# Optimization experiments

Hardware: AMD Instinct MI355X
Metric: run time of the kernel (lower is better)

The kernel has to match this reference:

```python
import jax, jax.numpy as jnp
import numpy as np

NUM_NODES = 20000
NUM_EDGES = 1_000_000
NUM_REL = 12        # internal num_relation (init arg 24 // 2)
NUM_STEP = 6
HID = 128
B_SET = 64          # number of unique (h, r) queries
BS, NEG = 64, 32    # scoring batch
EPS = 1e-10


def setup_inputs() -> dict:
    key = jax.random.key(0)
    ks = jax.random.split(key, 16)
    s = 0.1
    inp = {
        "query_emb": jax.random.normal(ks[0], (2 * NUM_REL + 1, HID), jnp.float32) * s,
        "w_ih": jax.random.normal(ks[1], (4 * HID, HID), jnp.float32) * s,
        "w_hh": jax.random.normal(ks[2], (4 * HID, HID), jnp.float32) * s,
        "b_ih": jax.random.normal(ks[3], (4 * HID,), jnp.float32) * s,
        "b_hh": jax.random.normal(ks[4], (4 * HID,), jnp.float32) * s,
        "wl_w": jax.random.normal(ks[5], (2 * NUM_REL, HID), jnp.float32) * s,
        "wl_b": jax.random.normal(ks[6], (2 * NUM_REL,), jnp.float32) * s,
        "lin_w": jax.random.normal(ks[7], (1, 1), jnp.float32),
        "lin_b": jax.random.normal(ks[8], (1,), jnp.float32),
        "edge_index": jax.random.randint(ks[9], (2, NUM_EDGES), 0, NUM_NODES, jnp.int64),
        "edge_type": jax.random.randint(ks[10], (NUM_EDGES,), 0, 2 * NUM_REL, jnp.int64),
        "h_set": jax.random.randint(ks[11], (B_SET,), 0, NUM_NODES, jnp.int64),
        "r_set": jax.random.randint(ks[12], (B_SET,), 0, NUM_REL, jnp.int64),
        "t_index": jax.random.randint(ks[13], (BS, NEG), 0, NUM_NODES, jnp.int64),
        "hr_inverse": jax.random.randint(ks[14], (BS, NEG), 0, B_SET, jnp.int64),
    }
    return inp


def _lstm(query, w_ih, w_hh, b_ih, b_hh):
    # query: [T, B, D]; single-layer PyTorch LSTM (gate order i, f, g, o)
    B, D = query.shape[1], w_hh.shape[1]
    h0 = jnp.zeros((B, D), query.dtype)

    def step(carry, x):
        h, c = carry
        gates = x @ w_ih.T + b_ih + h @ w_hh.T + b_hh
        i, f, g, o = jnp.split(gates, 4, axis=-1)
        c = jax.nn.sigmoid(f) * c + jax.nn.sigmoid(i) * jnp.tanh(g)
        h = jax.nn.sigmoid(o) * jnp.tanh(c)
        return (h, c), h

    _, hidden = jax.lax.scan(step, (h0, h0), query)
    return hidden  # [T, B, D]


def reference(query_emb, w_ih, w_hh, b_ih, b_hh, wl_w, wl_b, lin_w, lin_b,
              edge_index, edge_type, h_set, r_set, t_index, hr_inverse):
    N1 = NUM_NODES + 1
    B = h_set.shape[0]
    # query sequence: relation repeated (T-1) times, then END token (= NUM_REL)
    q_index = jnp.concatenate(
        [jnp.tile(r_set[None, :], (NUM_STEP - 1, 1)),
         jnp.full((1, B), NUM_REL, dtype=r_set.dtype)], axis=0)  # [T, B]
    query = query_emb[q_index]                                   # [T, B, D]
    hidden = _lstm(query, w_ih, w_hh, b_ih, b_hh)                # [T, B, D]

    memory = jax.nn.one_hot(h_set, N1, dtype=query_emb.dtype)[None]  # [1, B, N1]
    node_in, node_out = edge_index[0], edge_index[1]

    output = None
    for i in range(NUM_STEP):
        k = hidden[i]                 # [B, D]
        v = hidden[: i + 1]           # [i+1, B, D]
        attn = jax.nn.softmax(jnp.einsum('bd,tbd->bt', k, v), axis=-1)
        inp = jnp.einsum('bt,tbn->nb', attn, memory)             # [N1, B]
        weight = jax.nn.softmax(k @ wl_w.T + wl_b, axis=-1).T    # [2R, B]
        # gather -> weight -> scatter_add over edges (edge_weight == 1)
        message = inp[node_in] * weight[edge_type]               # [E, B]
        output = jax.ops.segment_sum(message, node_out, num_segments=N1)
        output = output / jnp.maximum(output.sum(0, keepdims=True), EPS)
        memory = jnp.concatenate([memory, output.T[None]], axis=0)

    score = output[t_index, hr_inverse]           # [BS, NEG]
    return score * lin_w[0, 0] + lin_b[0]
```

## Files before the change

### kernel.cpp

```cpp
#include <hip/hip_runtime.h>
#include <hip/hip_fp16.h>
#include <math.h>

namespace {

constexpr int kN1 = 20001;
constexpr int kNE = 1000000;
constexpr int kNStep = 6;
constexpr int kHid = 128;
constexpr int kB = 64;
constexpr int kNRel2 = 24;
constexpr float kEps = 1e-10f;
constexpr unsigned kSent = (unsigned)kN1;
constexpr int kPMax = kNE + 8 * kN1;
constexpr int kGatherBlocks = 2048;
constexpr int kNWaves = kGatherBlocks * 4;

__device__ __forceinline__ float sig(float x) { return 1.0f / (1.0f + expf(-x)); }

__device__ __forceinline__ float2 cvt2(unsigned u) {
  __half2 h = *reinterpret_cast<__half2*>(&u);
  return __half22float2(h);
}


__global__ __launch_bounds__(256) void transpose_w_kernel(
    const float* __restrict__ w_ih, const float* __restrict__ w_hh,
    float* __restrict__ wt) {
  const int idx = blockIdx.x * 256 + threadIdx.x;
  if (idx < 256 * 512) {
    const int k = idx >> 9;
    const int j = idx & 511;
    wt[idx] = (k < 128) ? w_ih[j * kHid + k] : w_hh[j * kHid + (k - 128)];
  }
}

__global__ __launch_bounds__(512) void lstm_fast_kernel(
    const float* __restrict__ query_emb, const float* __restrict__ wt,
    const float* __restrict__ b_ih, const float* __restrict__ b_hh,
    const int* __restrict__ r_set, float* __restrict__ hidden ) {
  const int b = blockIdx.x;
  const int tid = threadIdx.x;
  __shared__ float xh[256];
  __shared__ float cst[kHid];
  __shared__ float gsm[512];
  const float bias = b_ih[tid] + b_hh[tid];
  const int q = r_set[b];
  if (tid < kHid) { cst[tid] = 0.f; xh[kHid + tid] = 0.f; }
  for (int s = 0; s < kNStep; ++s) {
    if (tid < kHid) xh[tid] = query_emb[((s < kNStep - 1) ? q : 12) * kHid + tid];
    __syncthreads();
    float acc = bias;
#pragma unroll 8
    for (int k = 0; k < 256; ++k) acc += xh[k] * wt[k * 512 + tid];
    gsm[tid] = acc;
    __syncthreads();
    if (tid < kHid) {
      const float ig = sig(gsm[tid]);
      const float fg = sig(gsm[kHid + tid]);
      const float gg = tanhf(gsm[2 * kHid + tid]);
      const float og = sig(gsm[3 * kHid + tid]);
      const float cn = fg * cst[tid] + ig * gg;
      cst[tid] = cn;
      const float hn = og * tanhf(cn);
      xh[kHid + tid] = hn;
      hidden[(s * kB + b) * kHid + tid] = hn;
    }
    __syncthreads();
  }
}

__global__ __launch_bounds__(256) void lstm_kernel(
    const float* __restrict__ query_emb, const float* __restrict__ w_ih,
    const float* __restrict__ w_hh, const float* __restrict__ b_ih,
    const float* __restrict__ b_hh, const int* __restrict__ r_set,
    float* __restrict__ hidden) {
  const int b = blockIdx.x;
  const int tid = threadIdx.x;
  __shared__ float xs[kHid], hs[kHid], cs[kHid], gates[4 * kHid];
  if (tid < kHid) { hs[tid] = 0.f; cs[tid] = 0.f; }
  __syncthreads();
  for (int s = 0; s < kNStep; ++s) {
    const int q = (s < kNStep - 1) ? r_set[b] : 12;
    if (tid < kHid) xs[tid] = query_emb[q * kHid + tid];
    __syncthreads();
    for (int j = tid; j < 4 * kHid; j += blockDim.x) {
      const float* wi = &w_ih[j * kHid];
      const float* wh = &w_hh[j * kHid];
      float a = b_ih[j] + b_hh[j];
#pragma unroll 4
      for (int k = 0; k < kHid; ++k) a += xs[k] * wi[k] + hs[k] * wh[k];
      gates[j] = a;
    }
    __syncthreads();
    if (tid < kHid) {
      const float ig = sig(gates[tid]);
      const float fg = sig(gates[kHid + tid]);
      const float gg = tanhf(gates[2 * kHid + tid]);
      const float og = sig(gates[3 * kHid + tid]);
      const float cn = fg * cs[tid] + ig * gg;
      const float hn = og * tanhf(cn);
      cs[tid] = cn;
      hs[tid] = hn;
      hidden[(s * kB + b) * kHid + tid] = hn;
    }
    __syncthreads();
  }
}

__global__ __launch_bounds__(128) void attn_weight_kernel(
    const float* __restrict__ hidden, const float* __restrict__ wl_w,
    const float* __restrict__ wl_b, float* __restrict__ attnAll ,
    float* __restrict__ weightAll ) {
  const int b = blockIdx.x;
  const int tid = threadIdx.x;
  __shared__ float hsm[kNStep][kHid];
  __shared__ float G[kNStep][kNStep];
  __shared__ float logits[kNStep][kNRel2];
  for (int s = 0; s < kNStep; ++s) hsm[s][tid] = hidden[(s * kB + b) * kHid + tid];
  __syncthreads();
  if (tid < 36) {
    const int i = tid / 6, t = tid % 6;
    if (t <= i) {
      float acc = 0.f;
      for (int k = 0; k < kHid; ++k) acc += hsm[i][k] * hsm[t][k];
      G[i][t] = acc;
    }
  }
  for (int p = tid; p < kNStep * kNRel2; p += 128) {
    const int i = p / kNRel2, r = p % kNRel2;
    float acc = wl_b[r];
    for (int k = 0; k < kHid; ++k) acc += hsm[i][k] * wl_w[r * kHid + k];
    logits[i][r] = acc;
  }
  __syncthreads();
  if (tid < kNStep) {
    const int i = tid;
    float m = G[i][0];
    for (int t = 1; t <= i; ++t) m = fmaxf(m, G[i][t]);
    float ssum = 0.f;
    float ev[kNStep];
    for (int t = 0; t <= i; ++t) { ev[t] = expf(G[i][t] - m); ssum += ev[t]; }
    for (int t = 0; t <= i; ++t) attnAll[(i * kNStep + t) * kB + b] = ev[t] / ssum;
    float mw = logits[i][0];
    for (int r = 1; r < kNRel2; ++r) mw = fmaxf(mw, logits[i][r]);
    float sw = 0.f;
    float ew[kNRel2];
    for (int r = 0; r < kNRel2; ++r) { ew[r] = expf(logits[i][r] - mw); sw += ew[r]; }
    for (int r = 0; r < kNRel2; ++r) weightAll[(i * kNRel2 + r) * kB + b] = ew[r] / sw;
  }
}


__global__ __launch_bounds__(256) void zero_kernel(int* __restrict__ counts,
                                                   float* __restrict__ colsumAll) {
  const int i = blockIdx.x * blockDim.x + threadIdx.x;
  if (i < kN1) counts[i] = 0;
  if (i < kNStep * kB) colsumAll[i] = 0.f;
}

__global__ __launch_bounds__(256) void hist_kernel(const int* __restrict__ nout,
                                                   int* __restrict__ counts) {
  for (int e = blockIdx.x * blockDim.x + threadIdx.x; e < kNE;
       e += gridDim.x * blockDim.x)
    atomicAdd(&counts[nout[e]], 1);
}

__global__ __launch_bounds__(1024) void scan_kernel(const int* __restrict__ counts,
                                                    int* __restrict__ poffsets,
                                                    int* __restrict__ cursor) {
  __shared__ int part[1024];
  const int tid = threadIdx.x;
  const int chunk = (kN1 + 1023) / 1024;
  const int beg = tid * chunk;
  const int end = min(beg + chunk, kN1);
  int s = 0;
  for (int i = beg; i < end; ++i) s += (counts[i] + 7) & ~7;
  part[tid] = s;
  __syncthreads();
  for (int off = 1; off < 1024; off <<= 1) {
    const int v = (tid >= off) ? part[tid - off] : 0;
    __syncthreads();
    part[tid] += v;
    __syncthreads();
  }
  int run = part[tid] - s;
  for (int i = beg; i < end; ++i) {
    poffsets[i] = run;
    cursor[i] = run;
    run += (counts[i] + 7) & ~7;
  }
  if (tid == 1023) poffsets[kN1] = part[1023];
}

__global__ __launch_bounds__(256) void fill_kernel(unsigned* __restrict__ packed) {
  for (int i = blockIdx.x * blockDim.x + threadIdx.x; i < kPMax;
       i += gridDim.x * blockDim.x)
    packed[i] = kSent;
}

__global__ __launch_bounds__(256) void permute_kernel(
    const int* __restrict__ nin, const int* __restrict__ nout,
    const int* __restrict__ etype, int* __restrict__ cursor,
    unsigned* __restrict__ packed) {
  for (int e = blockIdx.x * blockDim.x + threadIdx.x; e < kNE;
       e += gridDim.x * blockDim.x) {
    const int d = nout[e];
    const int pos = atomicAdd(&cursor[d], 1);
    packed[pos] = (unsigned)nin[e] | ((unsigned)etype[e] << 15);
  }
}


__global__ __launch_bounds__(256) void inp_kernel(
    const float* __restrict__ attnAll, const float* __restrict__ colsumAll,
    const int* __restrict__ h_set, const float* __restrict__ outs,
    __half* __restrict__ inp, int step) {
  __shared__ float coef[kNStep][kB];
  __shared__ int hsm[kB];
  const int tid = threadIdx.x;
  for (int j = tid; j < kNStep * kB; j += 256) {
    const int t = j >> 6, b = j & 63;
    float c = 0.f;
    if (t == 0)
      c = attnAll[(step * kNStep) * kB + b];
    else if (t <= step)
      c = attnAll[(step * kNStep + t) * kB + b] /
          fmaxf(colsumAll[(t - 1) * kB + b], kEps);
    coef[t][b] = c;
  }
  if (tid < kB) hsm[tid] = h_set[tid];
  __syncthreads();
  const int total = (kN1 + 1) * 16;
  for (int idx = blockIdx.x * blockDim.x + tid; idx < total;
       idx += gridDim.x * blockDim.x) {
    const int n = idx >> 4;
    const int cg = idx & 15;
    float ax = 0.f, ay = 0.f, az = 0.f, aw = 0.f;
    if (n < kN1) {
      for (int t = 1; t <= step; ++t) {
        const float4 ct = *reinterpret_cast<const float4*>(&coef[t][cg * 4]);
        const float4 o = *reinterpret_cast<const float4*>(
            &outs[((long long)(t - 1) * kN1 + n) * kB + cg * 4]);
        ax += ct.x * o.x; ay += ct.y * o.y; az += ct.z * o.z; aw += ct.w * o.w;
      }
      const int c0 = cg * 4;
      if (hsm[c0 + 0] == n) ax += coef[0][c0 + 0];
      if (hsm[c0 + 1] == n) ay += coef[0][c0 + 1];
      if (hsm[c0 + 2] == n) az += coef[0][c0 + 2];
      if (hsm[c0 + 3] == n) aw += coef[0][c0 + 3];
    }
    __half2 h0 = __floats2half2_rn(ax, ay);
    __half2 h1 = __floats2half2_rn(az, aw);
    uint2 u;
    u.x = *reinterpret_cast<unsigned*>(&h0);
    u.y = *reinterpret_cast<unsigned*>(&h1);
    *reinterpret_cast<uint2*>(inp + (long long)idx * 4) = u;
  }
}

__global__ __launch_bounds__(256) void gather_seg_kernel(
    const __half* __restrict__ inp ,
    const float* __restrict__ weight ,
    const unsigned* __restrict__ packed, const int* __restrict__ poffsets,
    float* __restrict__ out, float* __restrict__ colsum) {
  __shared__ __align__(16) __half wsm[kNRel2 * kB];
  __shared__ float red[4][kB];
  const int tid = threadIdx.x;
  const int lane = tid & 63;
  const int wid = tid >> 6;
  const int g = lane >> 3;
  const int cb = lane & 7;
  for (int j = tid; j < kNRel2 * kB; j += 256) wsm[j] = __float2half(weight[j]);
  __syncthreads();

  float csum[8] = {0.f, 0.f, 0.f, 0.f, 0.f, 0.f, 0.f, 0.f};
  float acc[8] = {0.f, 0.f, 0.f, 0.f, 0.f, 0.f, 0.f, 0.f};

  auto flushNode = [&](int node) {
#pragma unroll
    for (int j = 0; j < 8; ++j) {
      acc[j] += __shfl_xor(acc[j], 8);
      acc[j] += __shfl_xor(acc[j], 16);
      acc[j] += __shfl_xor(acc[j], 32);
    }
    if (g == 0) {
      *reinterpret_cast<float4*>(out + (long long)node * kB + cb * 8) =
          make_float4(acc[0], acc[1], acc[2], acc[3]);
      *reinterpret_cast<float4*>(out + (long long)node * kB + cb * 8 + 4) =
          make_float4(acc[4], acc[5], acc[6], acc[7]);
#pragma unroll
      for (int j = 0; j < 8; ++j) csum[j] += acc[j];
    }
#pragma unroll
    for (int j = 0; j < 8; ++j) acc[j] = 0.f;
  };

  const int wave = blockIdx.x * 4 + wid;
  const int P = poffsets[kN1];
  const int nG = P >> 3;
  const int chunkG = (nG + kNWaves - 1) / kNWaves;
  const int gbeg = wave * chunkG;
  if (gbeg < nG) {
    const int gend = min(gbeg + chunkG, nG);
    auto lb = [&](int x) {
      int lo = 0, hi = kN1;
      while (lo < hi) {
        const int mid = (lo + hi) >> 1;
        if (poffsets[mid] < x) lo = mid + 1; else hi = mid;
      }
      return lo;
    };
    const int nbeg = lb(gbeg * 8);
    const int nend = (gend >= nG) ? kN1 : lb(gend * 8);
    if (nbeg < nend) {
      int n = nbeg;
      int nextB = poffsets[n + 1];
      const int ebeg = poffsets[nbeg];
      const int eend = poffsets[nend];
      unsigned pA = (ebeg < eend) ? packed[ebeg + g] : kSent;
      unsigned pB = (ebeg + 8 < eend) ? packed[ebeg + 8 + g] : kSent;
      uint4 vA = *reinterpret_cast<const uint4*>(
          inp + (long long)(pA & 0x7fffu) * kB + cb * 8);
      uint4 vB = *reinterpret_cast<const uint4*>(
          inp + (long long)(pB & 0x7fffu) * kB + cb * 8);
      for (int ebase = ebeg; ebase < eend; ebase += 16) {
        const bool hasB = (ebase + 8) < eend;
        const int e2 = ebase + 16, e3 = ebase + 24;
        const unsigned pC = (e2 < eend) ? packed[e2 + g] : kSent;
        const unsigned pD = (e3 < eend) ? packed[e3 + g] : kSent;
        while (ebase >= nextB) { flushNode(n); ++n; nextB = poffsets[n + 1]; }
        {
          const uint4 w4 =
              *reinterpret_cast<const uint4*>(wsm + (pA >> 15) * kB + cb * 8);
          const float2 v0 = cvt2(vA.x), v1 = cvt2(vA.y), v2 = cvt2(vA.z), v3 = cvt2(vA.w);
          const float2 w0 = cvt2(w4.x), w1 = cvt2(w4.y), w2 = cvt2(w4.z), w3 = cvt2(w4.w);
          acc[0] += v0.x * w0.x; acc[1] += v0.y * w0.y;
          acc[2] += v1.x * w1.x; acc[3] += v1.y * w1.y;
          acc[4] += v2.x * w2.x; acc[5] += v2.y * w2.y;
          acc[6] += v3.x * w3.x; acc[7] += v3.y * w3.y;
        }
        if (hasB) {
          while (ebase + 8 >= nextB) { flushNode(n); ++n; nextB = poffsets[n + 1]; }
          const uint4 w4 =
              *reinterpret_cast<const uint4*>(wsm + (pB >> 15) * kB + cb * 8);
          const float2 v0 = cvt2(vB.x), v1 = cvt2(vB.y), v2 = cvt2(vB.z), v3 = cvt2(vB.w);
          const float2 w0 = cvt2(w4.x), w1 = cvt2(w4.y), w2 = cvt2(w4.z), w3 = cvt2(w4.w);
          acc[0] += v0.x * w0.x; acc[1] += v0.y * w0.y;
          acc[2] += v1.x * w1.x; acc[3] += v1.y * w1.y;
          acc[4] += v2.x * w2.x; acc[5] += v2.y * w2.y;
          acc[6] += v3.x * w3.x; acc[7] += v3.y * w3.y;
        }
        pA = pC; pB = pD;
        vA = *reinterpret_cast<const uint4*>(
            inp + (long long)(pC & 0x7fffu) * kB + cb * 8);
        vB = *reinterpret_cast<const uint4*>(
            inp + (long long)(pD & 0x7fffu) * kB + cb * 8);
      }
      while (n < nend) { flushNode(n); ++n; }
    }
  }
  if (g == 0) {
#pragma unroll
    for (int j = 0; j < 8; ++j) red[wid][cb * 8 + j] = csum[j];
  }
  __syncthreads();
  if (wid == 0) {
    const float r = red[0][lane] + red[1][lane] + red[2][lane] + red[3][lane];
    unsafeAtomicAdd(&colsum[lane], r);
  }
}

__global__ __launch_bounds__(256) void score_kernel(
    const float* __restrict__ outLast, const float* __restrict__ colsumLast,
    const int* __restrict__ t_index, const int* __restrict__ hr_inverse,
    const float* __restrict__ lin_w, const float* __restrict__ lin_b,
    float* __restrict__ out, int n) {
  const int i = blockIdx.x * blockDim.x + threadIdx.x;
  if (i < n) {
    const int node = t_index[i];
    const int b = hr_inverse[i];
    const float v = outLast[(long long)node * kB + b] / fmaxf(colsumLast[b], kEps);
    out[i] = v * lin_w[0] + lin_b[0];
  }
}


__global__ __launch_bounds__(256) void inp_zero_kernel(
    const float* __restrict__ attnAll, const int* __restrict__ h_set,
    const float* __restrict__ outs, float* __restrict__ inp,
    float* __restrict__ out_next, float* __restrict__ colsum, int step) {
  const long long total = (long long)kN1 * kB;
  for (long long idx = (long long)blockIdx.x * blockDim.x + threadIdx.x; idx < total;
       idx += (long long)gridDim.x * blockDim.x) {
    const int b = (int)(idx & 63);
    const int n = (int)(idx >> 6);
    float acc = (h_set[b] == n) ? attnAll[(step * kNStep) * kB + b] : 0.f;
    for (int t = 1; t <= step; ++t)
      acc += attnAll[(step * kNStep + t) * kB + b] *
             outs[(long long)(t - 1) * kN1 * kB + idx];
    inp[idx] = acc;
    out_next[idx] = 0.f;
  }
  if (blockIdx.x == 0 && threadIdx.x < kB) colsum[threadIdx.x] = 0.f;
}

__global__ __launch_bounds__(256) void scatter_kernel(
    const float* __restrict__ inp, const float* __restrict__ weight,
    const int* __restrict__ nin, const int* __restrict__ nout,
    const int* __restrict__ etype, float* __restrict__ out,
    float* __restrict__ colsum) {
  const int lane = threadIdx.x & 63;
  const int wave = blockIdx.x * (blockDim.x >> 6) + (threadIdx.x >> 6);
  const int nwave = gridDim.x * (blockDim.x >> 6);
  __shared__ float wsm[kNRel2 * kB];
  for (int j = threadIdx.x; j < kNRel2 * kB; j += blockDim.x) wsm[j] = weight[j];
  __syncthreads();
  float csum = 0.f;
  for (int e = wave; e < kNE; e += nwave) {
    const float v = inp[(long long)nin[e] * kB + lane] * wsm[etype[e] * kB + lane];
    unsafeAtomicAdd(&out[(long long)nout[e] * kB + lane], v);
    csum += v;
  }
  unsafeAtomicAdd(&colsum[lane], csum);
}

__global__ __launch_bounds__(256) void normalize_kernel(
    float* __restrict__ out, const float* __restrict__ colsum) {
  const long long total = (long long)kN1 * kB;
  for (long long idx = (long long)blockIdx.x * blockDim.x + threadIdx.x; idx < total;
       idx += (long long)gridDim.x * blockDim.x)
    out[idx] /= fmaxf(colsum[idx & 63], kEps);
}

__global__ __launch_bounds__(256) void score_kernel_norm(
    const float* __restrict__ outLast, const int* __restrict__ t_index,
    const int* __restrict__ hr_inverse, const float* __restrict__ lin_w,
    const float* __restrict__ lin_b, float* __restrict__ out, int n) {
  const int i = blockIdx.x * blockDim.x + threadIdx.x;
  if (i < n) {
    out[i] = outLast[(long long)t_index[i] * kB + hr_inverse[i]] * lin_w[0] + lin_b[0];
  }
}

}

extern "C" void kernel_launch(void* const* d_in, const int* in_sizes, int n_in,
                              void* d_out, int out_size, void* d_ws, size_t ws_size,
                              hipStream_t stream) {
  const float* query_emb = (const float*)d_in[0];
  const float* w_ih = (const float*)d_in[1];
  const float* w_hh = (const float*)d_in[2];
  const float* b_ih = (const float*)d_in[3];
  const float* b_hh = (const float*)d_in[4];
  const float* wl_w = (const float*)d_in[5];
  const float* wl_b = (const float*)d_in[6];
  const float* lin_w = (const float*)d_in[7];
  const float* lin_b = (const float*)d_in[8];
  const int* edge_index = (const int*)d_in[9];
  const int* edge_type = (const int*)d_in[10];
  const int* h_set = (const int*)d_in[11];
  const int* r_set = (const int*)d_in[12];
  const int* t_index = (const int*)d_in[13];
  const int* hr_inverse = (const int*)d_in[14];
  float* out = (float*)d_out;

  const int* nin = edge_index;
  const int* nout = edge_index + kNE;

  float* ws = (float*)d_ws;
  float* hidden = ws;
  float* attnAll = hidden + kNStep * kB * kHid;
  float* weightAll = attnAll + kNStep * kNStep * kB;
  float* colsumAll = weightAll + kNStep * kNRel2 * kB;
  float* inpF32 = colsumAll + kNStep * kB;
  __half* inpH = (__half*)inpF32;
  float* outs = inpF32 + (long long)kN1 * kB;
  float* tail = outs + (long long)kNStep * kN1 * kB;
  int* counts = (int*)tail;
  int* poffsets = counts + kN1;
  int* cursor = poffsets + kN1 + 1;
  unsigned* packed = (unsigned*)(cursor + kN1);
  float* wt = (float*)(packed + kPMax);
  const size_t needed = (size_t)((char*)(wt + 256 * 512) - (char*)d_ws);

  if (ws_size >= needed) {
    transpose_w_kernel<<<512, 256, 0, stream>>>(w_ih, w_hh, wt);
    lstm_fast_kernel<<<kB, 512, 0, stream>>>(query_emb, wt, b_ih, b_hh, r_set, hidden);
    attn_weight_kernel<<<kB, 128, 0, stream>>>(hidden, wl_w, wl_b, attnAll, weightAll);

    zero_kernel<<<(kN1 + 255) / 256, 256, 0, stream>>>(counts, colsumAll);
    hist_kernel<<<1024, 256, 0, stream>>>(nout, counts);
    scan_kernel<<<1, 1024, 0, stream>>>(counts, poffsets, cursor);
    fill_kernel<<<1024, 256, 0, stream>>>(packed);
    permute_kernel<<<1024, 256, 0, stream>>>(nin, nout, edge_type, cursor, packed);

    const int inp_threads = (kN1 + 1) * 16;
    for (int i = 0; i < kNStep; ++i) {
      float* out_i = outs + (long long)i * kN1 * kB;
      inp_kernel<<<(inp_threads + 255) / 256, 256, 0, stream>>>(
          attnAll, colsumAll, h_set, outs, inpH, i);
      gather_seg_kernel<<<kGatherBlocks, 256, 0, stream>>>(
          inpH, weightAll + i * kNRel2 * kB, packed, poffsets, out_i,
          colsumAll + i * kB);
    }
    score_kernel<<<(out_size + 255) / 256, 256, 0, stream>>>(
        outs + 5LL * kN1 * kB, colsumAll + 5 * kB, t_index, hr_inverse, lin_w, lin_b,
        out, out_size);
  } else {
    lstm_kernel<<<kB, 256, 0, stream>>>(query_emb, w_ih, w_hh, b_ih, b_hh, r_set,
                                        hidden);
    attn_weight_kernel<<<kB, 128, 0, stream>>>(hidden, wl_w, wl_b, attnAll, weightAll);
    float* colsum = colsumAll;
    for (int i = 0; i < kNStep; ++i) {
      float* out_i = outs + (long long)i * kN1 * kB;
      inp_zero_kernel<<<2048, 256, 0, stream>>>(attnAll, h_set, outs, inpF32, out_i,
                                                colsum, i);
      scatter_kernel<<<4096, 256, 0, stream>>>(inpF32, weightAll + i * kNRel2 * kB,
                                               nin, nout, edge_type, out_i, colsum);
      normalize_kernel<<<2048, 256, 0, stream>>>(out_i, colsum);
    }
    score_kernel_norm<<<(out_size + 255) / 256, 256, 0, stream>>>(
        outs + 5LL * kN1 * kB, t_index, hr_inverse, lin_w, lin_b, out, out_size);
  }
}
```

Measured before the change: 669.7 us.

## Privatize CSR build counters per XCD, pad-only fill, prefetch inp, wave-wide index loads

The histogram and permute atomics now go to per-XCD sub-counters, which the scan reduces and turns into per-XCD cursors. This is meant to cut cross-die atomic contention. The full-buffer sentinel fill is replaced by a kernel that writes only the padding slots of each node. In the gather kernel, every block first streams a slice of the fp16 inp matrix to warm the L2, and packed edge indices are now loaded 64 at a time per wave and handed out by shuffles with a two-deep row prefetch. The cost is extra memory reads for the warm-up pass and more scan work.

```diff
diff --git a/kernel.cpp b/kernel.cpp
--- a/kernel.cpp
+++ b/kernel.cpp
@@ -15,6 +15,7 @@
 constexpr int kPMax = kNE + 8 * kN1;
 constexpr int kGatherBlocks = 2048;
 constexpr int kNWaves = kGatherBlocks * 4;
+constexpr int kNXcd = 8;
 
 __device__ __forceinline__ float sig(float x) { return 1.0f / (1.0f + expf(-x)); }
 
@@ -152,30 +153,37 @@
 }
 
 
-__global__ __launch_bounds__(256) void zero_kernel(int* __restrict__ counts,
+__global__ __launch_bounds__(256) void zero_kernel(int* __restrict__ count2,
                                                    float* __restrict__ colsumAll) {
   const int i = blockIdx.x * blockDim.x + threadIdx.x;
-  if (i < kN1) counts[i] = 0;
+  if (i < kN1 * kNXcd) count2[i] = 0;
   if (i < kNStep * kB) colsumAll[i] = 0.f;
 }
 
-__global__ __launch_bounds__(256) void hist_kernel(const int* __restrict__ nout,
-                                                   int* __restrict__ counts) {
+__global__ __launch_bounds__(256) void hist2_kernel(const int* __restrict__ nout,
+                                                    int* __restrict__ count2) {
+  const int xcd = blockIdx.x & (kNXcd - 1);
   for (int e = blockIdx.x * blockDim.x + threadIdx.x; e < kNE;
        e += gridDim.x * blockDim.x)
-    atomicAdd(&counts[nout[e]], 1);
-}
-
-__global__ __launch_bounds__(1024) void scan_kernel(const int* __restrict__ counts,
-                                                    int* __restrict__ poffsets,
-                                                    int* __restrict__ cursor) {
+    atomicAdd(&count2[nout[e] * kNXcd + xcd], 1);
+}
+
+__global__ __launch_bounds__(1024) void scan_kernel(int* __restrict__ count2,
+                                                    int* __restrict__ counts,
+                                                    int* __restrict__ poffsets) {
   __shared__ int part[1024];
   const int tid = threadIdx.x;
   const int chunk = (kN1 + 1023) / 1024;
   const int beg = tid * chunk;
   const int end = min(beg + chunk, kN1);
   int s = 0;
-  for (int i = beg; i < end; ++i) s += (counts[i] + 7) & ~7;
+  for (int i = beg; i < end; ++i) {
+    int c = 0;
+#pragma unroll
+    for (int x = 0; x < kNXcd; ++x) c += count2[i * kNXcd + x];
+    counts[i] = c;
+    s += (c + 7) & ~7;
+  }
   part[tid] = s;
   __syncthreads();
   for (int off = 1; off < 1024; off <<= 1) {
@@ -187,26 +195,38 @@
   int run = part[tid] - s;
   for (int i = beg; i < end; ++i) {
     poffsets[i] = run;
-    cursor[i] = run;
+    int sub = run;
+#pragma unroll
+    for (int x = 0; x < kNXcd; ++x) {
+      const int c = count2[i * kNXcd + x];
+      count2[i * kNXcd + x] = sub;
+      sub += c;
+    }
     run += (counts[i] + 7) & ~7;
   }
   if (tid == 1023) poffsets[kN1] = part[1023];
 }
 
-__global__ __launch_bounds__(256) void fill_kernel(unsigned* __restrict__ packed) {
-  for (int i = blockIdx.x * blockDim.x + threadIdx.x; i < kPMax;
-       i += gridDim.x * blockDim.x)
-    packed[i] = kSent;
+__global__ __launch_bounds__(256) void pad_fill_kernel(
+    const int* __restrict__ poffsets, const int* __restrict__ counts,
+    unsigned* __restrict__ packed) {
+  const int i = blockIdx.x * blockDim.x + threadIdx.x;
+  if (i < kN1) {
+    const int s = poffsets[i] + counts[i];
+    const int e = poffsets[i + 1];
+    for (int k = s; k < e; ++k) packed[k] = kSent;
+  }
 }
 
 __global__ __launch_bounds__(256) void permute_kernel(
     const int* __restrict__ nin, const int* __restrict__ nout,
-    const int* __restrict__ etype, int* __restrict__ cursor,
+    const int* __restrict__ etype, int* __restrict__ cursor2,
     unsigned* __restrict__ packed) {
+  const int xcd = blockIdx.x & (kNXcd - 1);
   for (int e = blockIdx.x * blockDim.x + threadIdx.x; e < kNE;
        e += gridDim.x * blockDim.x) {
     const int d = nout[e];
-    const int pos = atomicAdd(&cursor[d], 1);
+    const int pos = atomicAdd(&cursor2[d * kNXcd + xcd], 1);
     packed[pos] = (unsigned)nin[e] | ((unsigned)etype[e] << 15);
   }
 }
@@ -271,6 +291,16 @@
   const int wid = tid >> 6;
   const int g = lane >> 3;
   const int cb = lane & 7;
+  {
+    const uint4* base = reinterpret_cast<const uint4*>(inp);
+    const int tot = (kN1 + 1) * 8;
+    const int per = (tot + 255) / 256;
+    const int s0 = (blockIdx.x & 255) * per;
+    const int s1 = min(s0 + per, tot);
+    unsigned sink = 0;
+    for (int i = s0 + tid; i < s1; i += 256) sink ^= base[i].x;
+    asm volatile("" :: "v"(sink));
+  }
   for (int j = tid; j < kNRel2 * kB; j += 256) wsm[j] = __float2half(weight[j]);
   __syncthreads();
 
@@ -318,44 +348,43 @@
       int nextB = poffsets[n + 1];
       const int ebeg = poffsets[nbeg];
       const int eend = poffsets[nend];
-      unsigned pA = (ebeg < eend) ? packed[ebeg + g] : kSent;
-      unsigned pB = (ebeg + 8 < eend) ? packed[ebeg + 8 + g] : kSent;
-      uint4 vA = *reinterpret_cast<const uint4*>(
-          inp + (long long)(pA & 0x7fffu) * kB + cb * 8);
-      uint4 vB = *reinterpret_cast<const uint4*>(
-          inp + (long long)(pB & 0x7fffu) * kB + cb * 8);
-      for (int ebase = ebeg; ebase < eend; ebase += 16) {
-        const bool hasB = (ebase + 8) < eend;
-        const int e2 = ebase + 16, e3 = ebase + 24;
-        const unsigned pC = (e2 < eend) ? packed[e2 + g] : kSent;
-        const unsigned pD = (e3 < eend) ? packed[e3 + g] : kSent;
-        while (ebase >= nextB) { flushNode(n); ++n; nextB = poffsets[n + 1]; }
-        {
+      auto ld_pk = [&](int idx) -> unsigned {
+        const unsigned r = packed[idx];
+        return (idx < eend) ? r : kSent;
+      };
+      auto rowload = [&](unsigned p) -> uint4 {
+        return *reinterpret_cast<const uint4*>(
+            inp + (long long)(p & 0x7fffu) * kB + cb * 8);
+      };
+      unsigned pb = ld_pk(ebeg + lane);
+      unsigned p0 = __shfl(pb, g);
+      unsigned p1 = __shfl(pb, 8 + g);
+      uint4 v0 = rowload(p0);
+      uint4 v1 = rowload(p1);
+      for (int wbase = ebeg; wbase < eend; wbase += 64) {
+        const unsigned pbN = ld_pk(wbase + 64 + lane);
+#pragma unroll
+        for (int j = 0; j < 8; ++j) {
+          const int cur = wbase + j * 8;
+          if (cur >= eend) break;
+          const int jj = j + 2;
+          const unsigned p2 = (jj < 8) ? __shfl(pb, jj * 8 + g)
+                                       : __shfl(pbN, (jj - 8) * 8 + g);
+          const uint4 v2 = rowload(p2);
+          while (cur >= nextB) { flushNode(n); ++n; nextB = poffsets[n + 1]; }
           const uint4 w4 =
-              *reinterpret_cast<const uint4*>(wsm + (pA >> 15) * kB + cb * 8);
-          const float2 v0 = cvt2(vA.x), v1 = cvt2(vA.y), v2 = cvt2(vA.z), v3 = cvt2(vA.w);
-          const float2 w0 = cvt2(w4.x), w1 = cvt2(w4.y), w2 = cvt2(w4.z), w3 = cvt2(w4.w);
-          acc[0] += v0.x * w0.x; acc[1] += v0.y * w0.y;
-          acc[2] += v1.x * w1.x; acc[3] += v1.y * w1.y;
-          acc[4] += v2.x * w2.x; acc[5] += v2.y * w2.y;
-          acc[6] += v3.x * w3.x; acc[7] += v3.y * w3.y;
+              *reinterpret_cast<const uint4*>(wsm + (p0 >> 15) * kB + cb * 8);
+          const float2 a0 = cvt2(v0.x), a1 = cvt2(v0.y), a2 = cvt2(v0.z),
+                       a3 = cvt2(v0.w);
+          const float2 b0 = cvt2(w4.x), b1 = cvt2(w4.y), b2 = cvt2(w4.z),
+                       b3 = cvt2(w4.w);
+          acc[0] += a0.x * b0.x; acc[1] += a0.y * b0.y;
+          acc[2] += a1.x * b1.x; acc[3] += a1.y * b1.y;
+          acc[4] += a2.x * b2.x; acc[5] += a2.y * b2.y;
+          acc[6] += a3.x * b3.x; acc[7] += a3.y * b3.y;
+          p0 = p1; v0 = v1; p1 = p2; v1 = v2;
         }
-        if (hasB) {
-          while (ebase + 8 >= nextB) { flushNode(n); ++n; nextB = poffsets[n + 1]; }
-          const uint4 w4 =
-              *reinterpret_cast<const uint4*>(wsm + (pB >> 15) * kB + cb * 8);
-          const float2 v0 = cvt2(vB.x), v1 = cvt2(vB.y), v2 = cvt2(vB.z), v3 = cvt2(vB.w);
-          const float2 w0 = cvt2(w4.x), w1 = cvt2(w4.y), w2 = cvt2(w4.z), w3 = cvt2(w4.w);
-          acc[0] += v0.x * w0.x; acc[1] += v0.y * w0.y;
-          acc[2] += v1.x * w1.x; acc[3] += v1.y * w1.y;
-          acc[4] += v2.x * w2.x; acc[5] += v2.y * w2.y;
-          acc[6] += v3.x * w3.x; acc[7] += v3.y * w3.y;
-        }
-        pA = pC; pB = pD;
-        vA = *reinterpret_cast<const uint4*>(
-            inp + (long long)(pC & 0x7fffu) * kB + cb * 8);
-        vB = *reinterpret_cast<const uint4*>(
-            inp + (long long)(pD & 0x7fffu) * kB + cb * 8);
+        pb = pbN;
       }
       while (n < nend) { flushNode(n); ++n; }
     }
@@ -479,8 +508,8 @@
   float* tail = outs + (long long)kNStep * kN1 * kB;
   int* counts = (int*)tail;
   int* poffsets = counts + kN1;
-  int* cursor = poffsets + kN1 + 1;
-  unsigned* packed = (unsigned*)(cursor + kN1);
+  int* count2 = poffsets + kN1 + 1;
+  unsigned* packed = (unsigned*)(count2 + kN1 * kNXcd);
   float* wt = (float*)(packed + kPMax);
   const size_t needed = (size_t)((char*)(wt + 256 * 512) - (char*)d_ws);
 
@@ -489,11 +518,11 @@
     lstm_fast_kernel<<<kB, 512, 0, stream>>>(query_emb, wt, b_ih, b_hh, r_set, hidden);
     attn_weight_kernel<<<kB, 128, 0, stream>>>(hidden, wl_w, wl_b, attnAll, weightAll);
 
-    zero_kernel<<<(kN1 + 255) / 256, 256, 0, stream>>>(counts, colsumAll);
-    hist_kernel<<<1024, 256, 0, stream>>>(nout, counts);
-    scan_kernel<<<1, 1024, 0, stream>>>(counts, poffsets, cursor);
-    fill_kernel<<<1024, 256, 0, stream>>>(packed);
-    permute_kernel<<<1024, 256, 0, stream>>>(nin, nout, edge_type, cursor, packed);
+    zero_kernel<<<(kN1 * kNXcd + 255) / 256, 256, 0, stream>>>(count2, colsumAll);
+    hist2_kernel<<<1024, 256, 0, stream>>>(nout, count2);
+    scan_kernel<<<1, 1024, 0, stream>>>(count2, counts, poffsets);
+    pad_fill_kernel<<<(kN1 + 255) / 256, 256, 0, stream>>>(poffsets, counts, packed);
+    permute_kernel<<<1024, 256, 0, stream>>>(nin, nout, edge_type, count2, packed);
 
     const int inp_threads = (kN1 + 1) * 16;
     for (int i = 0; i < kNStep; ++i) {
```

After: 737.8 us. 10.2% more time.
